# Performance work log

Measured on AMD Instinct MI355X. Metric: run time of the kernel, lower is better.

Reference implementation:

```python
import jax, jax.numpy as jnp
import numpy as np
from jax import lax

GAMMA = 2.0
BLANK = 0
NEG = -1e30  # log-space 'zero'
T, B, C, L = 1000, 64, 256, 100


def setup_inputs() -> dict:
    key = jax.random.key(0)
    k1, k2 = jax.random.split(key)
    # valid log-probabilities, as produced by a model's log_softmax head
    log_probs = jax.nn.log_softmax(jax.random.normal(k1, (T, B, C), dtype=jnp.float32), axis=-1)
    # concatenated targets, blank (0) excluded as CTC requires
    targets = jax.random.randint(k2, (B * L,), 1, C, dtype=jnp.int32)
    input_lengths = jnp.full((B,), T, dtype=jnp.int32)
    target_lengths = jnp.full((B,), L, dtype=jnp.int32)
    return {"log_probs": log_probs, "targets": targets,
            "input_lengths": input_lengths, "target_lengths": target_lengths}


def _ctc_loss(log_probs, targets2d, input_lengths, target_lengths):
    # log_probs: (T,B,C); targets2d: (B,L). Returns per-sample NLL (B,).
    Tt, Bb, _ = log_probs.shape
    Ll = targets2d.shape[1]
    S = 2 * Ll + 1  # extended label sequence: blank interleaved
    ext = jnp.full((Bb, S), BLANK, dtype=jnp.int32).at[:, 1::2].set(targets2d)
    # emission log-probs for each extended symbol: (T,B,S)
    emit = jnp.take_along_axis(log_probs, jnp.broadcast_to(ext[None], (Tt, Bb, S)), axis=2)
    # skip-transition allowed where symbol is non-blank and differs from s-2
    allow2 = jnp.concatenate(
        [jnp.zeros((Bb, 2), bool), (ext[:, 2:] != BLANK) & (ext[:, 2:] != ext[:, :-2])], axis=1)

    def shiftk(a, k):
        return jnp.pad(a, ((0, 0), (k, 0)), constant_values=NEG)[:, :S]

    alpha0 = jnp.full((Bb, S), NEG, jnp.float32).at[:, 0].set(emit[0, :, 0]).at[:, 1].set(emit[0, :, 1])

    def step(alpha, e):
        a1 = shiftk(alpha, 1)
        a2 = jnp.where(allow2, shiftk(alpha, 2), NEG)
        m = jnp.maximum(jnp.maximum(alpha, a1), a2)
        new = m + jnp.log(jnp.exp(alpha - m) + jnp.exp(a1 - m) + jnp.exp(a2 - m)) + e
        return new, new

    _, rest = lax.scan(step, alpha0, emit[1:])
    alphas = jnp.concatenate([alpha0[None], rest], axis=0)  # (T,B,S)
    b = jnp.arange(Bb)
    last = alphas[input_lengths - 1, b]  # (B,S) at each sample's final step
    ll = jnp.logaddexp(last[b, 2 * target_lengths], last[b, 2 * target_lengths - 1])
    # zero_infinity=True semantics
    return jnp.where(ll > NEG / 2, -ll, 0.0)


def reference(log_probs, targets, input_lengths, target_lengths):
    targets2d = targets.reshape(B, L)
    loss = _ctc_loss(log_probs, targets2d, input_lengths, target_lengths)  # (B,)
    # focal weights: mean-over-time prob of each target symbol (computed under no_grad in torch)
    mean_probs = jnp.exp(log_probs).mean(axis=0)  # (B,C)
    target_probs = lax.stop_gradient(
        jnp.take_along_axis(mean_probs, targets2d, axis=1).reshape(-1))  # (B*L,)
    focal_weight = (1.0 - target_probs) ** GAMMA
    # torch broadcasting quirk: (total,) * (B,1) -> (B,total); mean over all
    return (focal_weight[None, :] * loss[:, None]).mean()
```

## Files before the change

### kernel.cpp

```cpp
#include <hip/hip_runtime.h>
#include <cstdint>

#define T_DIM 1000
#define B_DIM 64
#define C_DIM 256
#define L_DIM 100
#define S_DIM (2 * L_DIM + 1)
#define CH 32
#define NPROD 7
#define RPW 5

typedef float f32x4 __attribute__((ext_vector_type(4)));

#define DPP_I(x, ctrl) __builtin_amdgcn_update_dpp(0, (x), (ctrl), 0xF, 0xF, true)
#define DPP_F(x, ctrl) __int_as_float(DPP_I(__float_as_int(x), (ctrl)))

#define DSR(dst, addr, OFF) \
    asm volatile("ds_read_b32 %0, %1 offset:" OFF : "=v"(dst) : "v"(addr))
#define ISS(s, OFF) do { DSR(pb##s, apb, OFF); DSR(qa##s, aq1, OFF); DSR(qb##s, aq3, OFF); } while (0)
#define W(N) do { asm volatile("s_waitcnt lgkmcnt(" N ")"); __builtin_amdgcn_sched_barrier(0); } while (0)
#define STP(s) step(pb##s, qa##s, qb##s)

__device__ __forceinline__ float wave_max_dpp(float x) {
    x = fmaxf(x, DPP_F(x, 0x111));
    x = fmaxf(x, DPP_F(x, 0x112));
    x = fmaxf(x, DPP_F(x, 0x114));
    x = fmaxf(x, DPP_F(x, 0x118));
    x = fmaxf(x, DPP_F(x, 0x142));
    x = fmaxf(x, DPP_F(x, 0x143));
    return __int_as_float(__builtin_amdgcn_readlane(__float_as_int(x), 63));
}

__global__ __launch_bounds__(256) void mean_pass(
        const float* __restrict__ lp, float* __restrict__ ws_mean) {
    const int mb = blockIdx.x;
    const int b = mb >> 3;
    const int t0 = (mb & 7) * 125;
    const int lane = threadIdx.x & 63;
    const int wv = threadIdx.x >> 6;
    const uint32_t rstride = B_DIM * C_DIM;
    const float* p = lp + (size_t)b * C_DIM + (lane << 2);
    f32x4 s = {0.f, 0.f, 0.f, 0.f};
    for (int t = t0 + wv; t < t0 + 125; t += 4) {
        f32x4 v = *(const f32x4*)(p + (size_t)t * rstride);
        s.x += __expf(v.x); s.y += __expf(v.y);
        s.z += __expf(v.z); s.w += __expf(v.w);
    }
    __shared__ float sums[4][C_DIM];
    *(f32x4*)&sums[wv][lane << 2] = s;
    __syncthreads();
    const int c = threadIdx.x;
    const float tot = sums[0][c] + sums[1][c] + sums[2][c] + sums[3][c];
    atomicAdd(&ws_mean[b * C_DIM + c], tot * (1.0f / T_DIM));
}

__global__ __launch_bounds__(512, 1) void ctc_fused(
        const float* __restrict__ lp,
        const int* __restrict__ tgt,
        const int* __restrict__ il,
        const int* __restrict__ tl,
        float* __restrict__ ws_loss) {
    const int blk = blockIdx.x;
    const uint32_t rstride = B_DIM * C_DIM;

    __shared__ __align__(16) float rows[2][CH][C_DIM];

    const int tid = threadIdx.x;
    const int lane = tid & 63;
    const int wave = tid >> 6;
    const int b = blk;
    const int* trow = tgt + b * L_DIM;
    const int ilen = il[b];
    const int tlen = tl[b];

    const int i1 = 2 * lane;
    const int i3 = 2 * lane + 1;
    const int c1 = (i1 < L_DIM) ? trow[i1] : 0;
    const int c3 = (i3 < L_DIM) ? trow[i3] : 0;
    const int c1m = (i1 >= 1 && i1 - 1 < L_DIM) ? trow[i1 - 1] : -1;
    const float m1 = ((i1 >= 1) && (c1 != c1m)) ? 1.0f : 0.0f;
    const float m3 = (c3 != c1) ? 1.0f : 0.0f;

    const float f0 = (4 * lane + 0 < S_DIM) ? 1.0f : 0.0f;
    const float f1 = (4 * lane + 1 < S_DIM) ? 1.0f : 0.0f;
    const float f2 = (4 * lane + 2 < S_DIM) ? 1.0f : 0.0f;
    const float f3 = (4 * lane + 3 < S_DIM) ? 1.0f : 0.0f;

    const float* base = lp + (size_t)b * C_DIM;

    float a0 = 0.f, a1 = 0.f, a2 = 0.f, a3 = 0.f;
    {
        float i0 = __expf(base[0]);
        float i1v = __expf(base[c1]);
        if (lane == 0 && wave == 0) { a0 = i0; a1 = i1v; }
    }
    float ls = 0.f;

    auto produce = [&](int cc) {
        const int p = cc & 1;
        const int tstart = 1 + cc * CH;
        f32x4 v[RPW];
#pragma unroll
        for (int k = 0; k < RPW; ++k) {
            const int d = (wave - 1) + NPROD * k;
            if (d < CH) {
                int t = tstart + d; t = (t < ilen) ? t : (ilen - 1);
                v[k] = *(const f32x4*)(base + (size_t)t * rstride + (lane << 2));
            } else {
                v[k] = (f32x4){0.f, 0.f, 0.f, 0.f};
            }
        }
        asm volatile("" : "+v"(v[0]), "+v"(v[1]), "+v"(v[2]), "+v"(v[3]), "+v"(v[4]));
#pragma unroll
        for (int k = 0; k < RPW; ++k) {
            const int d = (wave - 1) + NPROD * k;
            if (d < CH) {
                f32x4 e;
                e.x = __expf(v[k].x); e.y = __expf(v[k].y);
                e.z = __expf(v[k].z); e.w = __expf(v[k].w);
                *(f32x4*)&rows[p][d][lane << 2] = e;
            }
        }
    };

    auto step = [&](float pb, float p1e, float p3e) {
        const float p3 = DPP_F(a3, 0x138);
        const float a01 = a0 + a1;
        const float n0 = (a0 + p3) * pb;
        const float n1 = fmaf(m1, p3, a01) * p1e;
        const float n2 = (a2 + a1) * pb;
        const float n3 = (fmaf(m3, a1, a2) + a3) * p3e;
        a0 = n0; a1 = n1; a2 = n2; a3 = n3;
    };

#define RENORM() do {                                                       \
        a0 *= f0; a1 *= f1; a2 *= f2; a3 *= f3;                             \
        const float mx = wave_max_dpp(fmaxf(fmaxf(a0, a1), fmaxf(a2, a3))); \
        const float inv = __builtin_amdgcn_rcpf(mx);                        \
        ls -= __logf(inv);                                                  \
        a0 *= inv; a1 *= inv; a2 *= inv; a3 *= inv;                         \
    } while (0)

    auto consume = [&](int cc) {
        const int p = cc & 1;
        const int tstart = 1 + cc * CH;
        if (tstart + CH <= ilen) {
            const uint32_t lbase =
                (uint32_t)(uintptr_t)(&rows[0][0][0]) + (uint32_t)(p * (CH * C_DIM * 4));
            uint32_t apb = lbase;
            uint32_t aq1 = lbase + ((uint32_t)c1 << 2);
            uint32_t aq3 = lbase + ((uint32_t)c3 << 2);
            float pb0, pb1, pb2, pb3, pb4;
            float qa0, qa1, qa2, qa3, qa4;
            float qb0, qb1, qb2, qb3, qb4;
            ISS(0, "0"); ISS(1, "1024"); ISS(2, "2048"); ISS(3, "3072"); ISS(4, "4096");
            W("12"); STP(0); ISS(0, "5120");
            W("12"); STP(1); ISS(1, "6144");
            W("12"); STP(2); ISS(2, "7168");
            W("12"); STP(3); ISS(3, "8192");
            W("12"); STP(4); ISS(4, "9216");
            W("12"); STP(0); ISS(0, "10240");
            W("12"); STP(1); ISS(1, "11264");
            W("12"); STP(2); ISS(2, "12288"); RENORM();
            W("12"); STP(3); ISS(3, "13312");
            W("12"); STP(4); ISS(4, "14336");
            W("12"); STP(0); ISS(0, "15360");
            W("12"); STP(1); ISS(1, "16384");
            W("12"); STP(2); ISS(2, "17408");
            W("12"); STP(3); ISS(3, "18432");
            W("12"); STP(4); ISS(4, "19456");
            W("12"); STP(0); ISS(0, "20480"); RENORM();
            W("12"); STP(1); ISS(1, "21504");
            W("12"); STP(2); ISS(2, "22528");
            W("12"); STP(3); ISS(3, "23552");
            W("12"); STP(4); ISS(4, "24576");
            W("12"); STP(0); ISS(0, "25600");
            W("12"); STP(1); ISS(1, "26624");
            W("12"); STP(2); ISS(2, "27648");
            W("12"); STP(3); ISS(3, "28672"); RENORM();
            W("12"); STP(4); ISS(4, "29696");
            W("12"); STP(0); ISS(0, "30720");
            W("12"); STP(1); ISS(1, "31744");
            W("12"); STP(2);
            W("9");  STP(3);
            W("6");  STP(4);
            W("3");  STP(0);
            W("0");  STP(1); RENORM();
        } else {
#pragma unroll
            for (int d = 0; d < CH; ++d) {
                if (tstart + d < ilen) {
                    step(rows[p][d][0], rows[p][d][c1], rows[p][d][c3]);
                    if ((d & 7) == 7) RENORM();
                }
            }
        }
    };

    const int nchunks = (ilen - 1 + CH - 1) / CH;
    if (wave != 0) produce(0);
    __syncthreads();
    if (wave == 0) __builtin_amdgcn_s_setprio(1);
    for (int c = 0; c < nchunks; ++c) {
        if (wave != 0) produce(c + 1);
        else consume(c);
        __syncthreads();
    }
    if (wave == 0) __builtin_amdgcn_s_setprio(0);
#undef RENORM

    if (wave != 0) return;

    const int s_hi = 2 * tlen;
    const int s_lo = 2 * tlen - 1;
    const int slot_hi = s_hi & 3, lane_hi = min(s_hi >> 2, 63);
    const int slot_lo = s_lo & 3, lane_lo = min(s_lo >> 2, 63);
    float ch = (slot_hi == 0) ? a0 : (slot_hi == 1) ? a1 : (slot_hi == 2) ? a2 : a3;
    float cl = (slot_lo == 0) ? a0 : (slot_lo == 1) ? a1 : (slot_lo == 2) ? a2 : a3;
    const float vh = __shfl(ch, lane_hi, 64);
    const float vl = __shfl(cl, lane_lo, 64);
    if (lane == 0) {
        const float s = vh + vl;
        const float loss = (s > 0.f) ? -(__logf(s) + ls) : 0.0f;
        ws_loss[b] = loss;
    }
}

__global__ __launch_bounds__(256) void ctc_finalize(
        const float* __restrict__ ws_mean, const float* __restrict__ ws_loss,
        const int* __restrict__ tgt, float* __restrict__ out) {
    const int tid = threadIdx.x;
    float fsum = 0.f;
#pragma unroll
    for (int k = 0; k < (B_DIM * L_DIM) / 256; ++k) {
        const int j = tid + k * 256;
        const int b = j / L_DIM;
        const int c = tgt[j];
        const float p = ws_mean[b * C_DIM + c];
        const float w = 1.0f - p;
        fsum += w * w;
    }
    float lsum = (tid < B_DIM) ? ws_loss[tid] : 0.f;
#pragma unroll
    for (int off = 32; off > 0; off >>= 1) {
        fsum += __shfl_down(fsum, off, 64);
        lsum += __shfl_down(lsum, off, 64);
    }
    __shared__ float sf[4], sl[4];
    const int w = tid >> 6;
    if ((tid & 63) == 0) { sf[w] = fsum; sl[w] = lsum; }
    __syncthreads();
    if (tid == 0) {
        const float F = sf[0] + sf[1] + sf[2] + sf[3];
        const float Lo = sl[0] + sl[1] + sl[2] + sl[3];
        out[0] = (F / (float)(B_DIM * L_DIM)) * (Lo / (float)B_DIM);
    }
}

extern "C" void kernel_launch(void* const* d_in, const int* in_sizes, int n_in,
                              void* d_out, int out_size, void* d_ws, size_t ws_size,
                              hipStream_t stream) {
    const float* lp = (const float*)d_in[0];
    const int* tgt = (const int*)d_in[1];
    const int* il = (const int*)d_in[2];
    const int* tl = (const int*)d_in[3];
    float* ws_mean = (float*)d_ws;
    float* ws_loss = ws_mean + B_DIM * C_DIM;

    hipMemsetAsync(ws_mean, 0, B_DIM * C_DIM * sizeof(float), stream);
    mean_pass<<<dim3(B_DIM * 8), dim3(256), 0, stream>>>(lp, ws_mean);
    ctc_fused<<<dim3(B_DIM), dim3(512), 0, stream>>>(lp, tgt, il, tl, ws_loss);
    ctc_finalize<<<dim3(1), dim3(256), 0, stream>>>(ws_mean, ws_loss, tgt, (float*)d_out);
}
```

Measured before the change: 149.1 us.

## Fuse mean pass into CTC kernel as extra blocks and double chunk size

Removes the separate mean_pass launch. Its exp-sum reduction now runs as 192 extra blocks of ctc_fused, placed on the CUs left idle by the 64 CTC blocks, so it overlaps with the serial alpha recursion. The CTC time-chunk size doubles from 32 to 64, with matching producer rows per wave and a longer unrolled LDS-read schedule. This halves the number of producer/consumer barriers. In exchange, shared memory per block and producer register pressure roughly double, and the mean blocks now compete for memory bandwidth with the CTC producers.

```diff
diff --git a/kernel.cpp b/kernel.cpp
--- a/kernel.cpp
+++ b/kernel.cpp
@@ -6,9 +6,10 @@
 #define C_DIM 256
 #define L_DIM 100
 #define S_DIM (2 * L_DIM + 1)
-#define CH 32
+#define CH 64
 #define NPROD 7
-#define RPW 5
+#define RPW 10
+#define MEAN_BLOCKS 192
 
 typedef float f32x4 __attribute__((ext_vector_type(4)));
 
@@ -20,6 +21,7 @@
 #define ISS(s, OFF) do { DSR(pb##s, apb, OFF); DSR(qa##s, aq1, OFF); DSR(qb##s, aq3, OFF); } while (0)
 #define W(N) do { asm volatile("s_waitcnt lgkmcnt(" N ")"); __builtin_amdgcn_sched_barrier(0); } while (0)
 #define STP(s) step(pb##s, qa##s, qb##s)
+#define SD(s, OFF) do { W("12"); STP(s); ISS(s, OFF); } while (0)
 
 __device__ __forceinline__ float wave_max_dpp(float x) {
     x = fmaxf(x, DPP_F(x, 0x111));
@@ -31,37 +33,42 @@
     return __int_as_float(__builtin_amdgcn_readlane(__float_as_int(x), 63));
 }
 
-__global__ __launch_bounds__(256) void mean_pass(
-        const float* __restrict__ lp, float* __restrict__ ws_mean) {
-    const int mb = blockIdx.x;
-    const int b = mb >> 3;
-    const int t0 = (mb & 7) * 125;
-    const int lane = threadIdx.x & 63;
-    const int wv = threadIdx.x >> 6;
-    const uint32_t rstride = B_DIM * C_DIM;
-    const float* p = lp + (size_t)b * C_DIM + (lane << 2);
-    f32x4 s = {0.f, 0.f, 0.f, 0.f};
-    for (int t = t0 + wv; t < t0 + 125; t += 4) {
-        f32x4 v = *(const f32x4*)(p + (size_t)t * rstride);
-        s.x += __expf(v.x); s.y += __expf(v.y);
-        s.z += __expf(v.z); s.w += __expf(v.w);
-    }
-    __shared__ float sums[4][C_DIM];
-    *(f32x4*)&sums[wv][lane << 2] = s;
-    __syncthreads();
-    const int c = threadIdx.x;
-    const float tot = sums[0][c] + sums[1][c] + sums[2][c] + sums[3][c];
-    atomicAdd(&ws_mean[b * C_DIM + c], tot * (1.0f / T_DIM));
-}
-
 __global__ __launch_bounds__(512, 1) void ctc_fused(
         const float* __restrict__ lp,
         const int* __restrict__ tgt,
         const int* __restrict__ il,
         const int* __restrict__ tl,
+        float* __restrict__ ws_mean,
         float* __restrict__ ws_loss) {
     const int blk = blockIdx.x;
     const uint32_t rstride = B_DIM * C_DIM;
+
+    if (blk >= B_DIM) {
+        __shared__ float sums[8][C_DIM];
+        const int mb = blk - B_DIM;
+        const int b = mb / 3;
+        const int slice = mb % 3;
+        const int start = slice * 336;
+        const int end = (slice == 2) ? T_DIM : start + 336;
+        const int lane = threadIdx.x & 63;
+        const int wv = threadIdx.x >> 6;
+        const float* p = lp + (size_t)b * C_DIM + (lane << 2);
+        f32x4 s = {0.f, 0.f, 0.f, 0.f};
+        for (int t = start + wv; t < end; t += 8) {
+            f32x4 v = *(const f32x4*)(p + (size_t)t * rstride);
+            s.x += __expf(v.x); s.y += __expf(v.y);
+            s.z += __expf(v.z); s.w += __expf(v.w);
+        }
+        *(f32x4*)&sums[wv][lane << 2] = s;
+        __syncthreads();
+        if (threadIdx.x < C_DIM) {
+            const int c = threadIdx.x;
+            float tot = sums[0][c] + sums[1][c] + sums[2][c] + sums[3][c]
+                      + sums[4][c] + sums[5][c] + sums[6][c] + sums[7][c];
+            atomicAdd(&ws_mean[b * C_DIM + c], tot * (1.0f / T_DIM));
+        }
+        return;
+    }
 
     __shared__ __align__(16) float rows[2][CH][C_DIM];
 
@@ -110,7 +117,8 @@
                 v[k] = (f32x4){0.f, 0.f, 0.f, 0.f};
             }
         }
-        asm volatile("" : "+v"(v[0]), "+v"(v[1]), "+v"(v[2]), "+v"(v[3]), "+v"(v[4]));
+        asm volatile("" : "+v"(v[0]), "+v"(v[1]), "+v"(v[2]), "+v"(v[3]), "+v"(v[4]),
+                          "+v"(v[5]), "+v"(v[6]), "+v"(v[7]), "+v"(v[8]), "+v"(v[9]));
 #pragma unroll
         for (int k = 0; k < RPW; ++k) {
             const int d = (wave - 1) + NPROD * k;
@@ -154,38 +162,70 @@
             float qa0, qa1, qa2, qa3, qa4;
             float qb0, qb1, qb2, qb3, qb4;
             ISS(0, "0"); ISS(1, "1024"); ISS(2, "2048"); ISS(3, "3072"); ISS(4, "4096");
-            W("12"); STP(0); ISS(0, "5120");
-            W("12"); STP(1); ISS(1, "6144");
-            W("12"); STP(2); ISS(2, "7168");
-            W("12"); STP(3); ISS(3, "8192");
-            W("12"); STP(4); ISS(4, "9216");
-            W("12"); STP(0); ISS(0, "10240");
-            W("12"); STP(1); ISS(1, "11264");
-            W("12"); STP(2); ISS(2, "12288"); RENORM();
-            W("12"); STP(3); ISS(3, "13312");
-            W("12"); STP(4); ISS(4, "14336");
-            W("12"); STP(0); ISS(0, "15360");
-            W("12"); STP(1); ISS(1, "16384");
-            W("12"); STP(2); ISS(2, "17408");
-            W("12"); STP(3); ISS(3, "18432");
-            W("12"); STP(4); ISS(4, "19456");
-            W("12"); STP(0); ISS(0, "20480"); RENORM();
-            W("12"); STP(1); ISS(1, "21504");
-            W("12"); STP(2); ISS(2, "22528");
-            W("12"); STP(3); ISS(3, "23552");
-            W("12"); STP(4); ISS(4, "24576");
-            W("12"); STP(0); ISS(0, "25600");
-            W("12"); STP(1); ISS(1, "26624");
-            W("12"); STP(2); ISS(2, "27648");
-            W("12"); STP(3); ISS(3, "28672"); RENORM();
-            W("12"); STP(4); ISS(4, "29696");
-            W("12"); STP(0); ISS(0, "30720");
-            W("12"); STP(1); ISS(1, "31744");
-            W("12"); STP(2);
-            W("9");  STP(3);
-            W("6");  STP(4);
-            W("3");  STP(0);
-            W("0");  STP(1); RENORM();
+            SD(0, "5120");
+            SD(1, "6144");
+            SD(2, "7168");
+            SD(3, "8192");
+            SD(4, "9216");
+            SD(0, "10240");
+            SD(1, "11264");
+            SD(2, "12288"); RENORM();
+            SD(3, "13312");
+            SD(4, "14336");
+            SD(0, "15360");
+            SD(1, "16384");
+            SD(2, "17408");
+            SD(3, "18432");
+            SD(4, "19456");
+            SD(0, "20480"); RENORM();
+            SD(1, "21504");
+            SD(2, "22528");
+            SD(3, "23552");
+            SD(4, "24576");
+            SD(0, "25600");
+            SD(1, "26624");
+            SD(2, "27648");
+            SD(3, "28672"); RENORM();
+            SD(4, "29696");
+            SD(0, "30720");
+            SD(1, "31744");
+            SD(2, "32768");
+            SD(3, "33792");
+            SD(4, "34816");
+            SD(0, "35840");
+            SD(1, "36864"); RENORM();
+            SD(2, "37888");
+            SD(3, "38912");
+            SD(4, "39936");
+            SD(0, "40960");
+            SD(1, "41984");
+            SD(2, "43008");
+            SD(3, "44032");
+            SD(4, "45056"); RENORM();
+            SD(0, "46080");
+            SD(1, "47104");
+            SD(2, "48128");
+            SD(3, "49152");
+            SD(4, "50176");
+            SD(0, "51200");
+            SD(1, "52224");
+            SD(2, "53248"); RENORM();
+            SD(3, "54272");
+            SD(4, "55296");
+            SD(0, "56320");
+            SD(1, "57344");
+            SD(2, "58368");
+            SD(3, "59392");
+            SD(4, "60416");
+            SD(0, "61440"); RENORM();
+            SD(1, "62464");
+            SD(2, "63488");
+            SD(3, "64512");
+            W("12"); STP(4);
+            W("9");  STP(0);
+            W("6");  STP(1);
+            W("3");  STP(2);
+            W("0");  STP(3); RENORM();
         } else {
 #pragma unroll
             for (int d = 0; d < CH; ++d) {
@@ -268,7 +308,7 @@
     float* ws_loss = ws_mean + B_DIM * C_DIM;
 
     hipMemsetAsync(ws_mean, 0, B_DIM * C_DIM * sizeof(float), stream);
-    mean_pass<<<dim3(B_DIM * 8), dim3(256), 0, stream>>>(lp, ws_mean);
-    ctc_fused<<<dim3(B_DIM), dim3(512), 0, stream>>>(lp, tgt, il, tl, ws_loss);
+    ctc_fused<<<dim3(B_DIM + MEAN_BLOCKS), dim3(512), 0, stream>>>(
+        lp, tgt, il, tl, ws_mean, ws_loss);
     ctc_finalize<<<dim3(1), dim3(256), 0, stream>>>(ws_mean, ws_loss, tgt, (float*)d_out);
 }
```

Measured after the change: 137.4 us. -7.8%, faster.

## Fuse mean pass into CTC kernel and stage only gathered emissions in LDS

Applied to the files above, without the earlier changes.

Removes the separate mean_pass launch. Extra blocks appended to the CTC grid now compute the per-batch mean probabilities, so that work overlaps the serial CTC recursion on otherwise idle CUs. Producer waves now gather only the blank and the two target-label log-probs per lane, and exponentiate only those, instead of the full 256-class row. They store the results in a compact 132-wide emission buffer, which cuts LDS footprint and the consumer's bank-conflicting indexed reads. The trade-off is scattered global gathers in place of coalesced vector loads, plus a longer-lived kernel that mixes two roles in one launch.

```diff
diff --git a/kernel.cpp b/kernel.cpp
--- a/kernel.cpp
+++ b/kernel.cpp
@@ -9,6 +9,8 @@
 #define CH 32
 #define NPROD 7
 #define RPW 5
+#define EMW 132
+#define MEAN_BLOCKS 192
 
 typedef float f32x4 __attribute__((ext_vector_type(4)));
 
@@ -20,6 +22,7 @@
 #define ISS(s, OFF) do { DSR(pb##s, apb, OFF); DSR(qa##s, aq1, OFF); DSR(qb##s, aq3, OFF); } while (0)
 #define W(N) do { asm volatile("s_waitcnt lgkmcnt(" N ")"); __builtin_amdgcn_sched_barrier(0); } while (0)
 #define STP(s) step(pb##s, qa##s, qb##s)
+#define SD(s, OFF) do { W("12"); STP(s); ISS(s, OFF); } while (0)
 
 __device__ __forceinline__ float wave_max_dpp(float x) {
     x = fmaxf(x, DPP_F(x, 0x111));
@@ -31,39 +34,44 @@
     return __int_as_float(__builtin_amdgcn_readlane(__float_as_int(x), 63));
 }
 
-__global__ __launch_bounds__(256) void mean_pass(
-        const float* __restrict__ lp, float* __restrict__ ws_mean) {
-    const int mb = blockIdx.x;
-    const int b = mb >> 3;
-    const int t0 = (mb & 7) * 125;
-    const int lane = threadIdx.x & 63;
-    const int wv = threadIdx.x >> 6;
-    const uint32_t rstride = B_DIM * C_DIM;
-    const float* p = lp + (size_t)b * C_DIM + (lane << 2);
-    f32x4 s = {0.f, 0.f, 0.f, 0.f};
-    for (int t = t0 + wv; t < t0 + 125; t += 4) {
-        f32x4 v = *(const f32x4*)(p + (size_t)t * rstride);
-        s.x += __expf(v.x); s.y += __expf(v.y);
-        s.z += __expf(v.z); s.w += __expf(v.w);
-    }
-    __shared__ float sums[4][C_DIM];
-    *(f32x4*)&sums[wv][lane << 2] = s;
-    __syncthreads();
-    const int c = threadIdx.x;
-    const float tot = sums[0][c] + sums[1][c] + sums[2][c] + sums[3][c];
-    atomicAdd(&ws_mean[b * C_DIM + c], tot * (1.0f / T_DIM));
-}
-
 __global__ __launch_bounds__(512, 1) void ctc_fused(
         const float* __restrict__ lp,
         const int* __restrict__ tgt,
         const int* __restrict__ il,
         const int* __restrict__ tl,
+        float* __restrict__ ws_mean,
         float* __restrict__ ws_loss) {
     const int blk = blockIdx.x;
     const uint32_t rstride = B_DIM * C_DIM;
 
-    __shared__ __align__(16) float rows[2][CH][C_DIM];
+    if (blk >= B_DIM) {
+        __shared__ float sums[8][C_DIM];
+        const int mb = blk - B_DIM;
+        const int b = mb / 3;
+        const int slice = mb % 3;
+        const int start = slice * 336;
+        const int end = (slice == 2) ? T_DIM : start + 336;
+        const int lane = threadIdx.x & 63;
+        const int wv = threadIdx.x >> 6;
+        const float* p = lp + (size_t)b * C_DIM + (lane << 2);
+        f32x4 s = {0.f, 0.f, 0.f, 0.f};
+        for (int t = start + wv; t < end; t += 8) {
+            f32x4 v = *(const f32x4*)(p + (size_t)t * rstride);
+            s.x += __expf(v.x); s.y += __expf(v.y);
+            s.z += __expf(v.z); s.w += __expf(v.w);
+        }
+        *(f32x4*)&sums[wv][lane << 2] = s;
+        __syncthreads();
+        if (threadIdx.x < C_DIM) {
+            const int c = threadIdx.x;
+            float tot = sums[0][c] + sums[1][c] + sums[2][c] + sums[3][c]
+                      + sums[4][c] + sums[5][c] + sums[6][c] + sums[7][c];
+            atomicAdd(&ws_mean[b * C_DIM + c], tot * (1.0f / T_DIM));
+        }
+        return;
+    }
+
+    __shared__ __align__(16) float emit[2][CH][EMW];
 
     const int tid = threadIdx.x;
     const int lane = tid & 63;
@@ -99,26 +107,34 @@
     auto produce = [&](int cc) {
         const int p = cc & 1;
         const int tstart = 1 + cc * CH;
-        f32x4 v[RPW];
+        const int w = wave - 1;
+        float v1[RPW], v3[RPW], v0[RPW];
 #pragma unroll
         for (int k = 0; k < RPW; ++k) {
-            const int d = (wave - 1) + NPROD * k;
+            const int d = w + NPROD * k;
             if (d < CH) {
                 int t = tstart + d; t = (t < ilen) ? t : (ilen - 1);
-                v[k] = *(const f32x4*)(base + (size_t)t * rstride + (lane << 2));
+                const float* rp = base + (size_t)t * rstride;
+                v1[k] = rp[c1];
+                v3[k] = rp[c3];
+                v0[k] = rp[0];
             } else {
-                v[k] = (f32x4){0.f, 0.f, 0.f, 0.f};
+                v1[k] = 0.f; v3[k] = 0.f; v0[k] = 0.f;
             }
         }
-        asm volatile("" : "+v"(v[0]), "+v"(v[1]), "+v"(v[2]), "+v"(v[3]), "+v"(v[4]));
+        asm volatile("" : "+v"(v1[0]), "+v"(v1[1]), "+v"(v1[2]), "+v"(v1[3]), "+v"(v1[4]),
+                          "+v"(v3[0]), "+v"(v3[1]), "+v"(v3[2]), "+v"(v3[3]), "+v"(v3[4]),
+                          "+v"(v0[0]), "+v"(v0[1]), "+v"(v0[2]), "+v"(v0[3]), "+v"(v0[4]));
 #pragma unroll
         for (int k = 0; k < RPW; ++k) {
-            const int d = (wave - 1) + NPROD * k;
+            const int d = w + NPROD * k;
             if (d < CH) {
-                f32x4 e;
-                e.x = __expf(v[k].x); e.y = __expf(v[k].y);
-                e.z = __expf(v[k].z); e.w = __expf(v[k].w);
-                *(f32x4*)&rows[p][d][lane << 2] = e;
+                const float e1 = __expf(v1[k]);
+                const float e3 = __expf(v3[k]);
+                const float e0 = __expf(v0[k]);
+                emit[p][d][lane] = e1;
+                emit[p][d][64 + lane] = e3;
+                if (lane == 0) emit[p][d][128] = e0;
             }
         }
     };
@@ -146,41 +162,41 @@
         const int tstart = 1 + cc * CH;
         if (tstart + CH <= ilen) {
             const uint32_t lbase =
-                (uint32_t)(uintptr_t)(&rows[0][0][0]) + (uint32_t)(p * (CH * C_DIM * 4));
-            uint32_t apb = lbase;
-            uint32_t aq1 = lbase + ((uint32_t)c1 << 2);
-            uint32_t aq3 = lbase + ((uint32_t)c3 << 2);
+                (uint32_t)(uintptr_t)(&emit[0][0][0]) + (uint32_t)(p * (CH * EMW * 4));
+            uint32_t apb = lbase + 512;
+            uint32_t aq1 = lbase + ((uint32_t)lane << 2);
+            uint32_t aq3 = aq1 + 256;
             float pb0, pb1, pb2, pb3, pb4;
             float qa0, qa1, qa2, qa3, qa4;
             float qb0, qb1, qb2, qb3, qb4;
-            ISS(0, "0"); ISS(1, "1024"); ISS(2, "2048"); ISS(3, "3072"); ISS(4, "4096");
-            W("12"); STP(0); ISS(0, "5120");
-            W("12"); STP(1); ISS(1, "6144");
-            W("12"); STP(2); ISS(2, "7168");
-            W("12"); STP(3); ISS(3, "8192");
-            W("12"); STP(4); ISS(4, "9216");
-            W("12"); STP(0); ISS(0, "10240");
-            W("12"); STP(1); ISS(1, "11264");
-            W("12"); STP(2); ISS(2, "12288"); RENORM();
-            W("12"); STP(3); ISS(3, "13312");
-            W("12"); STP(4); ISS(4, "14336");
-            W("12"); STP(0); ISS(0, "15360");
-            W("12"); STP(1); ISS(1, "16384");
-            W("12"); STP(2); ISS(2, "17408");
-            W("12"); STP(3); ISS(3, "18432");
-            W("12"); STP(4); ISS(4, "19456");
-            W("12"); STP(0); ISS(0, "20480"); RENORM();
-            W("12"); STP(1); ISS(1, "21504");
-            W("12"); STP(2); ISS(2, "22528");
-            W("12"); STP(3); ISS(3, "23552");
-            W("12"); STP(4); ISS(4, "24576");
-            W("12"); STP(0); ISS(0, "25600");
-            W("12"); STP(1); ISS(1, "26624");
-            W("12"); STP(2); ISS(2, "27648");
-            W("12"); STP(3); ISS(3, "28672"); RENORM();
-            W("12"); STP(4); ISS(4, "29696");
-            W("12"); STP(0); ISS(0, "30720");
-            W("12"); STP(1); ISS(1, "31744");
+            ISS(0, "0"); ISS(1, "528"); ISS(2, "1056"); ISS(3, "1584"); ISS(4, "2112");
+            SD(0, "2640");
+            SD(1, "3168");
+            SD(2, "3696");
+            SD(3, "4224");
+            SD(4, "4752");
+            SD(0, "5280");
+            SD(1, "5808");
+            SD(2, "6336"); RENORM();
+            SD(3, "6864");
+            SD(4, "7392");
+            SD(0, "7920");
+            SD(1, "8448");
+            SD(2, "8976");
+            SD(3, "9504");
+            SD(4, "10032");
+            SD(0, "10560"); RENORM();
+            SD(1, "11088");
+            SD(2, "11616");
+            SD(3, "12144");
+            SD(4, "12672");
+            SD(0, "13200");
+            SD(1, "13728");
+            SD(2, "14256");
+            SD(3, "14784"); RENORM();
+            SD(4, "15312");
+            SD(0, "15840");
+            SD(1, "16368");
             W("12"); STP(2);
             W("9");  STP(3);
             W("6");  STP(4);
@@ -190,7 +206,7 @@
 #pragma unroll
             for (int d = 0; d < CH; ++d) {
                 if (tstart + d < ilen) {
-                    step(rows[p][d][0], rows[p][d][c1], rows[p][d][c3]);
+                    step(emit[p][d][128], emit[p][d][lane], emit[p][d][64 + lane]);
                     if ((d & 7) == 7) RENORM();
                 }
             }
@@ -268,7 +284,7 @@
     float* ws_loss = ws_mean + B_DIM * C_DIM;
 
     hipMemsetAsync(ws_mean, 0, B_DIM * C_DIM * sizeof(float), stream);
-    mean_pass<<<dim3(B_DIM * 8), dim3(256), 0, stream>>>(lp, ws_mean);
-    ctc_fused<<<dim3(B_DIM), dim3(512), 0, stream>>>(lp, tgt, il, tl, ws_loss);
+    ctc_fused<<<dim3(B_DIM + MEAN_BLOCKS), dim3(512), 0, stream>>>(
+        lp, tgt, il, tl, ws_mean, ws_loss);
     ctc_finalize<<<dim3(1), dim3(256), 0, stream>>>(ws_mean, ws_loss, tgt, (float*)d_out);
 }
```

New measurement: 136.7 us. 8.3% less time.
